# Performance work log

Hardware: AMD Instinct MI355X
Metric: run time of the kernel (lower is better)

## Reference

```python
import jax, jax.numpy as jnp
import numpy as np

B, H, W = 64, 224, 224
EPS = 1e-5


def setup_inputs() -> dict:
    key = jax.random.key(0)
    ks = jax.random.split(key, 8)
    n = lambda k, s, std: jax.random.normal(k, s, jnp.float32) * std
    return {
        "x": jax.random.normal(ks[0], (B, 1, H, W), jnp.float32),
        "conv1_w": n(ks[1], (24, 1, 3, 3), 0.2),
        "conv1_b": jnp.zeros((24,), jnp.float32),
        "bn1_g": jnp.ones((24,), jnp.float32),
        "bn1_b": jnp.zeros((24,), jnp.float32),
        "conv2_w": n(ks[2], (48, 24, 3, 3), 0.07),
        "conv2_b": jnp.zeros((48,), jnp.float32),
        "bn2_g": jnp.ones((48,), jnp.float32),
        "bn2_b": jnp.zeros((48,), jnp.float32),
        "fconv_w": n(ks[3], (48, 48, 56, 56), 0.003),
        "fconv_b": jnp.zeros((48,), jnp.float32),
        "lin1_w": n(ks[4], (24, 48), 0.02),
        "lin1_b": jnp.zeros((24,), jnp.float32),
        "lin2_w": n(ks[5], (4, 24), 0.01),
        "lin2_b": jnp.array([0.0, 0.0, 1.0, 0.0], jnp.float32),  # torch init: identity transform bias
    }


def conv2d(x, w, b):
    y = jax.lax.conv_general_dilated(x, w, (1, 1), ((1, 1), (1, 1)),
                                     dimension_numbers=("NCHW", "OIHW", "NCHW"))
    return y + b[None, :, None, None]


def batchnorm(x, g, b):
    # train-mode BN: batch statistics over (N, H, W), biased variance
    m = x.mean((0, 2, 3), keepdims=True)
    v = x.var((0, 2, 3), keepdims=True)
    return (x - m) * jax.lax.rsqrt(v + EPS) * g[None, :, None, None] + b[None, :, None, None]


def maxpool2(x):
    b, c, h, w = x.shape
    return x.reshape(b, c, h // 2, 2, w // 2, 2).max(axis=(3, 5))


def affine_grid(theta, h, w):
    # theta: [B,2,3]; align_corners=False normalized coords (torch default)
    xs = (jnp.arange(w, dtype=jnp.float32) * 2 + 1) / w - 1.0
    ys = (jnp.arange(h, dtype=jnp.float32) * 2 + 1) / h - 1.0
    gx, gy = jnp.meshgrid(xs, ys)                      # [H,W] each
    base = jnp.stack([gx, gy, jnp.ones_like(gx)], -1)  # [H,W,3] (x, y, 1)
    return jnp.einsum("bij,hwj->bhwi", theta, base)    # [B,H,W,2] -> (x, y)


def grid_sample(img, grid):
    # bilinear, zeros padding, align_corners=False (torch defaults)
    b, c, h, w = img.shape
    ix = ((grid[..., 0] + 1.0) * w - 1.0) * 0.5        # [B,H,W]
    iy = ((grid[..., 1] + 1.0) * h - 1.0) * 0.5
    x0 = jnp.floor(ix); y0 = jnp.floor(iy)
    x1 = x0 + 1.0; y1 = y0 + 1.0
    wx1 = ix - x0; wx0 = 1.0 - wx1
    wy1 = iy - y0; wy0 = 1.0 - wy1
    bidx = jnp.arange(b)[:, None, None]

    def tap(xf, yf, wgt):
        valid = (xf >= 0) & (xf < w) & (yf >= 0) & (yf < h)
        xi = jnp.clip(xf, 0, w - 1).astype(jnp.int32)
        yi = jnp.clip(yf, 0, h - 1).astype(jnp.int32)
        vals = img[bidx, :, yi, xi]                    # [B,H,W,C]
        return vals * (wgt * valid)[..., None]

    out = (tap(x0, y0, wx0 * wy0) + tap(x1, y0, wx1 * wy0)
           + tap(x0, y1, wx0 * wy1) + tap(x1, y1, wx1 * wy1))
    return jnp.transpose(out, (0, 3, 1, 2))            # [B,C,H,W]


def reference(x, conv1_w, conv1_b, bn1_g, bn1_b, conv2_w, conv2_b, bn2_g, bn2_b,
              fconv_w, fconv_b, lin1_w, lin1_b, lin2_w, lin2_b):
    b, _, h, w = x.shape
    x1 = maxpool2(jax.nn.relu(batchnorm(conv2d(x, conv1_w, conv1_b), bn1_g, bn1_b)))
    x1 = maxpool2(jax.nn.relu(batchnorm(conv2d(x1, conv2_w, conv2_b), bn2_g, bn2_b)))
    # final_conv with kernel 56 over a 56x56 map == full contraction
    feat = jnp.einsum("bchw,ochw->bo", x1, fconv_w) + fconv_b      # [B,48]
    theta4 = jax.nn.relu(feat @ lin1_w.T + lin1_b) @ lin2_w.T + lin2_b  # [B,4]
    tx, ty, scale, angle = theta4[:, 0], theta4[:, 1], theta4[:, 2], theta4[:, 3]
    c, s = jnp.cos(angle), jnp.sin(angle)
    # (T @ R @ S)[:, :2] built directly, fully vectorized over batch
    row0 = jnp.stack([scale * c, -scale * s, tx], -1)
    row1 = jnp.stack([scale * s, scale * c, ty], -1)
    theta = jnp.stack([row0, row1], 1)                 # [B,2,3]
    grid = affine_grid(theta, h, w)
    out = grid_sample(x, grid)
    return out, tx, ty, scale, angle
```

## Files before the change

### kernel.cpp

```cpp
#include <hip/hip_runtime.h>
#include <hip/hip_bf16.h>

#define NB 64
#define H0 224
#define W0 224
#define C1 24
#define C2 48
#define H1 112
#define W1 112
#define H2 56
#define W2 56
#define EPSV 1e-5f

#define WS_STATS1   0
#define WS_STATS2   432
#define WS_FEAT     1296
#define WS_B2       4368
#define WS_X2       11280
#define WS_FWT      (WS_X2 + 4818944)
#define WS_X1       9645072
#define WS_NEED_BIG ((size_t)(WS_X1 + 9633792) * 4)
#define OUT0_ELEMS  (NB*H0*W0)

typedef _Float16 v8h __attribute__((ext_vector_type(8)));
typedef float    v4f __attribute__((ext_vector_type(4)));

static __device__ __forceinline__ unsigned short f2h(float v) {
    _Float16 h = (_Float16)v;
    unsigned short us;
    __builtin_memcpy(&us, &h, 2);
    return us;
}

__global__ __launch_bounds__(256) void k_stats_prep(
    const float* __restrict__ x, const float* __restrict__ w1, const float* __restrict__ b1,
    const float* __restrict__ w2, const float* __restrict__ fw,
    float* __restrict__ ws, _Float16* __restrict__ x1g, _Float16* __restrict__ fwt)
{
    __shared__ __align__(16) unsigned char smem[18432];
    const int tid = threadIdx.x;
    const int bid = blockIdx.x;

    if (bid >= 3136) {
        _Float16 (*T)[136] = (_Float16(*)[136])smem;
        const int p = bid - 3136;
        if (p < 54) {
            int t = p * 256 + tid;
            if (t >= 432 && t < WS_B2) ws[t] = 0.f;
            if (t < 13824) {
                int e = t & 7;
                int l = (t >> 3) & 63;
                int g = t >> 9;
                int q = l >> 4, ml = l & 15;
                int kp = g / 3, nt = g % 3;
                int ic = q * 8 + e;
                int oc = nt * 16 + ml;
                float v = (ic < C1) ? w2[(oc * C1 + ic) * 9 + kp] : 0.f;
                ((_Float16*)(ws + WS_B2))[t] = (_Float16)v;
            }
        }
        const int kb = p * 128;
#pragma unroll
        for (int t3 = 0; t3 < 6; t3++) {
            int li = tid + 256 * t3;
            int o = li >> 5, k4 = li & 31;
            float4 v = *(const float4*)&fw[(long)o * 150528 + kb + 4 * k4];
            T[o][4 * k4 + 0] = (_Float16)v.x;
            T[o][4 * k4 + 1] = (_Float16)v.y;
            T[o][4 * k4 + 2] = (_Float16)v.z;
            T[o][4 * k4 + 3] = (_Float16)v.w;
        }
        __syncthreads();
        uint4* dst = (uint4*)&fwt[(long)kb * 48];
#pragma unroll
        for (int t3 = 0; t3 < 3; t3++) {
            int u = tid + 256 * t3;
            int gg = u / 384;
            int rem = u % 384;
            int o = rem >> 3;
            int k8 = (rem & 7) * 8;
            dst[u] = *(const uint4*)&T[o][gg * 64 + k8];
        }
        return;
    }

    float (*xt)[36] = (float(*)[36])smem;
    unsigned int (*outt)[13] = (unsigned int(*)[13])(smem + 4896);
    float* sred = (float*)(smem + 18208);

    const int b = bid / 49;
    const int rem0 = bid % 49;
    const int py0 = (rem0 / 7) * 16, px0 = (rem0 % 7) * 16;
    const int iy0 = 2 * py0 - 1, ix0 = 2 * px0 - 1;
    const float* xb = x + b * (H0 * W0);

    for (int li = tid; li < 34 * 34; li += 256) {
        int ry = li / 34, rx = li % 34;
        int gy = iy0 + ry, gx = ix0 + rx;
        bool ok = (gy >= 0) & (gy < H0) & (gx >= 0) & (gx < W0);
        xt[ry][rx] = ok ? xb[gy * W0 + gx] : 0.f;
    }

    const int wid = tid >> 6;
    const int lane = tid & 63;
    const int c0 = wid * 6;

    const int c0s = __builtin_amdgcn_readfirstlane(c0);
    const float* __restrict__ wps = w1 + c0s * 9;
    float wr[54], br[6];
#pragma unroll
    for (int k = 0; k < 54; k++) wr[k] = wps[k];
#pragma unroll
    for (int c = 0; c < 6; c++) br[c] = b1[c0s + c];

    __syncthreads();

    float s[6] = {0.f, 0.f, 0.f, 0.f, 0.f, 0.f};
    float q[6] = {0.f, 0.f, 0.f, 0.f, 0.f, 0.f};
    const int pc = lane & 15;
    const int pr0 = lane >> 4;

#pragma unroll
    for (int pp = 0; pp < 4; pp++) {
        const int pr = pr0 + 4 * pp;
        float patch[16];
#pragma unroll
        for (int i2 = 0; i2 < 4; i2++)
#pragma unroll
            for (int j2 = 0; j2 < 4; j2++)
                patch[i2 * 4 + j2] = xt[2 * pr + i2][2 * pc + j2];

        unsigned int pk[3];
#pragma unroll
        for (int cp = 0; cp < 3; cp++) {
            unsigned int pv = 0;
#pragma unroll
            for (int h = 0; h < 2; h++) {
                int c = 2 * cp + h;
                float m4 = -1e30f;
#pragma unroll
                for (int sy = 0; sy < 2; sy++)
#pragma unroll
                    for (int sx = 0; sx < 2; sx++) {
                        float a = br[c];
#pragma unroll
                        for (int ky = 0; ky < 3; ky++)
#pragma unroll
                            for (int kx = 0; kx < 3; kx++)
                                a = fmaf(patch[(sy + ky) * 4 + (sx + kx)], wr[c * 9 + ky * 3 + kx], a);
                        s[c] += a;
                        q[c] = fmaf(a, a, q[c]);
                        m4 = fmaxf(m4, a);
                    }
                pv |= ((unsigned int)f2h(m4)) << (16 * h);
            }
            pk[cp] = pv;
        }
        int pos = pr * 16 + pc;
        outt[pos][wid * 3 + 0] = pk[0];
        outt[pos][wid * 3 + 1] = pk[1];
        outt[pos][wid * 3 + 2] = pk[2];
    }

#pragma unroll
    for (int c = 0; c < 6; c++) {
#pragma unroll
        for (int off = 32; off > 0; off >>= 1) {
            s[c] += __shfl_down(s[c], off, 64);
            q[c] += __shfl_down(q[c], off, 64);
        }
    }
    if (lane == 0) {
#pragma unroll
        for (int c = 0; c < 6; c++) {
            sred[c0 + c] = s[c];
            sred[C1 + c0 + c] = q[c];
        }
    }
    __syncthreads();

    if (tid < 2 * C1) {
        atomicAdd(&ws[WS_STATS1 + (bid & 7) * 2 * C1 + tid], sred[tid]);
    }

    for (int u = tid; u < 768; u += 256) {
        int pos = u / 3, prt = u % 3;
        int pr = pos >> 4, pcc = pos & 15;
        long p = (long)(b * H1 + (py0 + pr)) * W1 + (px0 + pcc);
        uint4 v;
        v.x = outt[pos][4 * prt + 0];
        v.y = outt[pos][4 * prt + 1];
        v.z = outt[pos][4 * prt + 2];
        v.w = outt[pos][4 * prt + 3];
        *(uint4*)(x1g + p * C1 + prt * 8) = v;
    }
}

__global__ __launch_bounds__(256, 2) void k_conv2_fused6(
    const _Float16* __restrict__ x1g, const _Float16* __restrict__ bpp,
    const float* __restrict__ g1, const float* __restrict__ bb1,
    const float* __restrict__ b2,
    float* __restrict__ ws, unsigned int* __restrict__ pooltu)
{
    __shared__ __align__(16) _Float16 x1t[2][18][18][32];
    __shared__ float alds[C1], bflds[C1];
    __shared__ float sred[2 * C2];

    const int tid = threadIdx.x;
    const int w = tid >> 6;
    const int lane = tid & 63;
    const int ml = lane & 15;
    const int qq = lane >> 4;

    v8h B[9][3];
#pragma unroll
    for (int kp = 0; kp < 9; kp++)
#pragma unroll
        for (int nt = 0; nt < 3; nt++)
            B[kp][nt] = *(const v8h*)&bpp[((kp * 3 + nt) * 64 + lane) * 8];

    if (tid < C1) {
        float s = 0.f, q = 0.f;
#pragma unroll
        for (int i = 0; i < 8; i++) {
            s += ws[WS_STATS1 + i * 2 * C1 + tid];
            q += ws[WS_STATS1 + i * 2 * C1 + C1 + tid];
        }
        const float N = (float)(NB * H0 * W0);
        float m = s / N;
        float v = q / N - m * m;
        float a = g1[tid] / sqrtf(v + EPSV);
        alds[tid] = a;
        bflds[tid] = bb1[tid] - m * a;
    }
    if (tid < 2 * C2) sred[tid] = 0.f;

    {
        v8h z8;
#pragma unroll
        for (int e = 0; e < 8; e++) z8[e] = (_Float16)0.f;
        for (int li = tid; li < 2 * 18 * 18; li += 256) {
            int bu = li / 324, pos = li % 324;
            *(v8h*)&x1t[bu][pos / 18][pos % 18][24] = z8;
        }
    }

    float bias[3] = {b2[ml], b2[16 + ml], b2[32 + ml]};

    int spart[4], spr[4], spc[4]; bool sv[4];
#pragma unroll
    for (int s4 = 0; s4 < 4; s4++) {
        int li = tid + s4 * 256;
        sv[s4] = li < 972;
        int part = li % 3;
        int pos = li / 3;
        spart[s4] = part;
        spr[s4] = pos / 18;
        spc[s4] = pos % 18;
    }

    const int nb = gridDim.x;
    const int NTILE = 3136;
    int qn = NTILE / nb, rn = NTILE % nb;
    int start = (blockIdx.x < rn) ? blockIdx.x * (qn + 1)
                                  : rn * (qn + 1) + (blockIdx.x - rn) * qn;
    int cnt = (blockIdx.x < rn) ? qn + 1 : qn;

    float svacc[3] = {0.f, 0.f, 0.f}, qvacc[3] = {0.f, 0.f, 0.f};

    v8h raw[4];
    bool inb_n[4];
    {
        int t = start;
        int tb = t / 49, rem = t % 49;
        int ty = (rem / 7) * 16, txx = (rem % 7) * 16;
#pragma unroll
        for (int s4 = 0; s4 < 4; s4++) {
#pragma unroll
            for (int e = 0; e < 8; e++) raw[s4][e] = (_Float16)0.f;
            int gy = ty - 1 + spr[s4], gx = txx - 1 + spc[s4];
            inb_n[s4] = sv[s4] & (gy >= 0) & (gy < H1) & (gx >= 0) & (gx < W1);
            if (inb_n[s4])
                raw[s4] = *(const v8h*)&x1g[((tb * H1 + gy) * W1 + gx) * C1 + spart[s4] * 8];
        }
    }
    __syncthreads();

#pragma unroll
    for (int s4 = 0; s4 < 4; s4++) {
        if (sv[s4]) {
            v8h r8;
            if (inb_n[s4]) {
#pragma unroll
                for (int e = 0; e < 8; e++) {
                    int c = spart[s4] * 8 + e;
                    float vv = fmaxf(fmaf((float)raw[s4][e], alds[c], bflds[c]), 0.f);
                    r8[e] = (_Float16)vv;
                }
            } else {
#pragma unroll
                for (int e = 0; e < 8; e++) r8[e] = (_Float16)0.f;
            }
            *(v8h*)&x1t[0][spr[s4]][spc[s4]][spart[s4] * 8] = r8;
        }
    }
    __syncthreads();

    for (int it = 0; it < cnt; it++) {
        const int cur = it & 1;
        const int t = start + it;
        const int tb = t / 49, rem = t % 49;
        const int ty = (rem / 7) * 16, txx = (rem % 7) * 16;

        const bool haveNext = (it + 1 < cnt);
        if (haveNext) {
            int t2 = t + 1;
            int nb2 = t2 / 49, rem2 = t2 % 49;
            int ny = (rem2 / 7) * 16, nx = (rem2 % 7) * 16;
#pragma unroll
            for (int s4 = 0; s4 < 4; s4++) {
#pragma unroll
                for (int e = 0; e < 8; e++) raw[s4][e] = (_Float16)0.f;
                int gy = ny - 1 + spr[s4], gx = nx - 1 + spc[s4];
                inb_n[s4] = sv[s4] & (gy >= 0) & (gy < H1) & (gx >= 0) & (gx < W1);
                if (inb_n[s4])
                    raw[s4] = *(const v8h*)&x1g[((nb2 * H1 + gy) * W1 + gx) * C1 + spart[s4] * 8];
            }
        }

        v4f acc[4][3];
#pragma unroll
        for (int mt = 0; mt < 4; mt++)
#pragma unroll
            for (int nt = 0; nt < 3; nt++)
                acc[mt][nt] = (v4f){0.f, 0.f, 0.f, 0.f};

#pragma unroll
        for (int kp = 0; kp < 9; kp++) {
            const int ky = kp / 3, kx = kp % 3;
#pragma unroll
            for (int mt = 0; mt < 4; mt++) {
                const int r = 4 * w + mt;
                v8h a = *(const v8h*)&x1t[cur][r + ky][ml + kx][qq * 8];
                acc[mt][0] = __builtin_amdgcn_mfma_f32_16x16x32_f16(a, B[kp][0], acc[mt][0], 0, 0, 0);
                acc[mt][1] = __builtin_amdgcn_mfma_f32_16x16x32_f16(a, B[kp][1], acc[mt][1], 0, 0, 0);
                acc[mt][2] = __builtin_amdgcn_mfma_f32_16x16x32_f16(a, B[kp][2], acc[mt][2], 0, 0, 0);
            }
        }

#pragma unroll
        for (int nt = 0; nt < 3; nt++) {
            int oc = nt * 16 + ml;
            float z[4][4];
#pragma unroll
            for (int mt = 0; mt < 4; mt++)
#pragma unroll
                for (int rg = 0; rg < 4; rg++) {
                    float val = acc[mt][nt][rg] + bias[nt];
                    z[mt][rg] = val;
                    svacc[nt] += val;
                    qvacc[nt] = fmaf(val, val, qvacc[nt]);
                }
#pragma unroll
            for (int h = 0; h < 2; h++) {
                int py = (ty >> 1) + 2 * w + h;
                float m0 = fmaxf(fmaxf(z[2 * h][0], z[2 * h][1]),
                                 fmaxf(z[2 * h + 1][0], z[2 * h + 1][1]));
                float m1 = fmaxf(fmaxf(z[2 * h][2], z[2 * h][3]),
                                 fmaxf(z[2 * h + 1][2], z[2 * h + 1][3]));
                int px0 = (txx >> 1) + qq * 2;
                int k = oc * 3136 + py * W2 + px0;
                unsigned int pk2 = (unsigned int)f2h(m0) | ((unsigned int)f2h(m1) << 16);
                pooltu[(((k >> 6) * NB + tb) << 5) + ((k & 63) >> 1)] = pk2;
            }
        }

        if (haveNext) {
#pragma unroll
            for (int s4 = 0; s4 < 4; s4++) {
                if (sv[s4]) {
                    v8h r8;
                    if (inb_n[s4]) {
#pragma unroll
                        for (int e = 0; e < 8; e++) {
                            int c = spart[s4] * 8 + e;
                            float vv = fmaxf(fmaf((float)raw[s4][e], alds[c], bflds[c]), 0.f);
                            r8[e] = (_Float16)vv;
                        }
                    } else {
#pragma unroll
                        for (int e = 0; e < 8; e++) r8[e] = (_Float16)0.f;
                    }
                    *(v8h*)&x1t[cur ^ 1][spr[s4]][spc[s4]][spart[s4] * 8] = r8;
                }
            }
        }
        __syncthreads();
    }

#pragma unroll
    for (int nt = 0; nt < 3; nt++) {
        float sv2 = svacc[nt], qv = qvacc[nt];
        sv2 += __shfl_xor(sv2, 16, 64); qv += __shfl_xor(qv, 16, 64);
        sv2 += __shfl_xor(sv2, 32, 64); qv += __shfl_xor(qv, 32, 64);
        if (qq == 0) {
            atomicAdd(&sred[nt * 16 + ml], sv2);
            atomicAdd(&sred[C2 + nt * 16 + ml], qv);
        }
    }
    __syncthreads();
    if (tid < 2 * C2) {
        atomicAdd(&ws[WS_STATS2 + (blockIdx.x & 7) * 2 * C2 + tid], sred[tid]);
    }
}

__global__ __launch_bounds__(256) void k_fconv6(
    const unsigned int* __restrict__ pooltu, const _Float16* __restrict__ fwt,
    const float* __restrict__ ws, const float* __restrict__ g2, const float* __restrict__ bb2,
    float* __restrict__ feat)
{
    __shared__ __align__(16) _Float16 fwh[48][136];
    __shared__ __align__(16) _Float16 x2h[64][136];
    __shared__ float csh[2 * C2];

    const int tid = threadIdx.x;
    const int bx = blockIdx.x;

    const uint4* fsrc = (const uint4*)fwt + (long)bx * 768;
    const uint4* psrc = (const uint4*)pooltu + (long)bx * 1024;
    uint4 fr[3], pr[4];
#pragma unroll
    for (int t3 = 0; t3 < 3; t3++) fr[t3] = fsrc[tid + 256 * t3];
#pragma unroll
    for (int t4 = 0; t4 < 4; t4++) pr[t4] = psrc[tid + 256 * t4];

    if (tid < C2) {
        int c = tid;
        float s = 0.f, q = 0.f;
#pragma unroll
        for (int i = 0; i < 8; i++) {
            s += ws[WS_STATS2 + i * 2 * C2 + c];
            q += ws[WS_STATS2 + i * 2 * C2 + C2 + c];
        }
        const float N = (float)(NB * H1 * W1);
        float m = s / N;
        float v = q / N - m * m;
        float a = g2[c] / sqrtf(v + EPSV);
        csh[c] = a;
        csh[C2 + c] = bb2[c] - m * a;
    }
    __syncthreads();

#pragma unroll
    for (int t3 = 0; t3 < 3; t3++) {
        int li = tid + 256 * t3;
        int gg = li / 384;
        int o = (li % 384) / 8;
        int kin = (li & 7) * 8;
        *(uint4*)&fwh[o][gg * 64 + kin] = fr[t3];
    }
    const int c0 = (2 * bx) / 49, c1 = (2 * bx + 1) / 49;
    const float a0 = csh[c0], bf0 = csh[C2 + c0];
    const float a1 = csh[c1], bf1 = csh[C2 + c1];
#pragma unroll
    for (int t4 = 0; t4 < 4; t4++) {
        int li = tid + 256 * t4;
        int gg = li >> 9;
        int b = (li & 511) >> 3;
        int kin = (li & 7) * 8;
        float aa = gg ? a1 : a0;
        float bb = gg ? bf1 : bf0;
        union { uint4 u; v8h h; } cv;
        cv.u = pr[t4];
        v8h r8;
#pragma unroll
        for (int e = 0; e < 8; e++)
            r8[e] = (_Float16)fmaxf(fmaf((float)cv.h[e], aa, bb), 0.f);
        *(v8h*)&x2h[b][gg * 64 + kin] = r8;
    }
    __syncthreads();

    const int w = tid >> 6;
    const int lane = tid & 63;
    const int ml = lane & 15;
    const int qq = lane >> 4;

    v4f acc[3];
#pragma unroll
    for (int ot = 0; ot < 3; ot++) acc[ot] = (v4f){0.f, 0.f, 0.f, 0.f};

#pragma unroll
    for (int ks = 0; ks < 4; ks++) {
        v8h a = *(const v8h*)&x2h[w * 16 + ml][ks * 32 + qq * 8];
#pragma unroll
        for (int ot = 0; ot < 3; ot++) {
            v8h bb = *(const v8h*)&fwh[ot * 16 + ml][ks * 32 + qq * 8];
            acc[ot] = __builtin_amdgcn_mfma_f32_16x16x32_f16(a, bb, acc[ot], 0, 0, 0);
        }
    }

#pragma unroll
    for (int ot = 0; ot < 3; ot++)
#pragma unroll
        for (int rg = 0; rg < 4; rg++)
            atomicAdd(&feat[(w * 16 + qq * 4 + rg) * C2 + ot * 16 + ml], acc[ot][rg]);
}

__global__ __launch_bounds__(256) void k_sample4(
    const float* __restrict__ x, const float* __restrict__ feat, const float* __restrict__ fcb,
    const float* __restrict__ l1w, const float* __restrict__ l1b,
    const float* __restrict__ l2w, const float* __restrict__ l2b,
    float* __restrict__ out)
{
    __shared__ float hsh[24];
    __shared__ float th[4];
    const int b = blockIdx.y;
    const int tid = threadIdx.x;
    if (tid < 24) {
        float a = l1b[tid];
#pragma unroll
        for (int o = 0; o < C2; o++)
            a = fmaf(feat[b * C2 + o] + fcb[o], l1w[tid * C2 + o], a);
        hsh[tid] = fmaxf(a, 0.f);
    }
    __syncthreads();
    if (tid < 4) {
        float a = l2b[tid];
#pragma unroll
        for (int jj = 0; jj < 24; jj++) a = fmaf(hsh[jj], l2w[tid * 24 + jj], a);
        th[tid] = a;
        if (blockIdx.x == 0) out[OUT0_ELEMS + tid * NB + b] = a;
    }
    __syncthreads();

    const float tx = th[0], ty = th[1], sc = th[2], an = th[3];
    const float cc = cosf(an), ss = sinf(an);
    const float t00 = sc * cc, t01 = -sc * ss, t10 = sc * ss, t11 = sc * cc;
    const float* xb = x + b * (H0 * W0);

    int idx = (blockIdx.x * 256 + tid) * 2;
    int i = idx / W0, j = idx % W0;
    float ys = (2.f * (float)i + 1.f) / (float)H0 - 1.f;

    float o2[2];
#pragma unroll
    for (int px = 0; px < 2; px++) {
        float xs = (2.f * (float)(j + px) + 1.f) / (float)W0 - 1.f;
        float gx = t00 * xs + t01 * ys + tx;
        float gy = t10 * xs + t11 * ys + ty;
        float ix = ((gx + 1.f) * (float)W0 - 1.f) * 0.5f;
        float iy = ((gy + 1.f) * (float)H0 - 1.f) * 0.5f;
        float x0 = floorf(ix), y0 = floorf(iy);
        float x1f = x0 + 1.f, y1f = y0 + 1.f;
        float wx1 = ix - x0, wx0 = 1.f - wx1;
        float wy1 = iy - y0, wy0 = 1.f - wy1;
        auto tap = [&](float xf, float yf, float wgt) -> float {
            bool valid = (xf >= 0.f) & (xf < (float)W0) & (yf >= 0.f) & (yf < (float)H0);
            int xi = (int)fminf(fmaxf(xf, 0.f), (float)(W0 - 1));
            int yi = (int)fminf(fmaxf(yf, 0.f), (float)(H0 - 1));
            return valid ? xb[yi * W0 + xi] * wgt : 0.f;
        };
        o2[px] = tap(x0, y0, wx0 * wy0) + tap(x1f, y0, wx1 * wy0)
               + tap(x0, y1f, wx0 * wy1) + tap(x1f, y1f, wx1 * wy1);
    }
    *(float2*)&out[(b * H0 + i) * W0 + j] = make_float2(o2[0], o2[1]);
}

__global__ __launch_bounds__(256) void k_init(const float* __restrict__ w2, float* __restrict__ ws)
{
    int t = blockIdx.x * 256 + threadIdx.x;
    if (t < WS_B2) ws[t] = 0.f;
    if (t < 13824) {
        int e = t & 7;
        int l = (t >> 3) & 63;
        int g = t >> 9;
        int q = l >> 4, ml = l & 15;
        int kp = g / 3, nt = g % 3;
        int ic = q * 8 + e;
        int oc = nt * 16 + ml;
        float v = (ic < C1) ? w2[(oc * C1 + ic) * 9 + kp] : 0.f;
        ((_Float16*)(ws + WS_B2))[t] = (_Float16)v;
    }
}

__global__ __launch_bounds__(256) void k_conv1_stats(
    const float* __restrict__ x, const float* __restrict__ w1, const float* __restrict__ b1,
    float* __restrict__ ws)
{
    float s[C1], q[C1];
#pragma unroll
    for (int c = 0; c < C1; c++) { s[c] = 0.f; q[c] = 0.f; }
    const int NT = gridDim.x * 256;
    const int total = NB * H0 * W0;
    for (int p = blockIdx.x * 256 + threadIdx.x; p < total; p += NT) {
        int b = p / (H0 * W0);
        int r = p % (H0 * W0);
        int y = r / W0;
        int xx = r % W0;
        const float* xb = x + b * (H0 * W0);
        float patch[9];
#pragma unroll
        for (int dy = 0; dy < 3; dy++)
#pragma unroll
            for (int dx = 0; dx < 3; dx++) {
                int yy = y + dy - 1, xc = xx + dx - 1;
                bool ok = (yy >= 0) & (yy < H0) & (xc >= 0) & (xc < W0);
                patch[dy * 3 + dx] = ok ? xb[yy * W0 + xc] : 0.f;
            }
#pragma unroll
        for (int c = 0; c < C1; c++) {
            const float* wp = w1 + c * 9;
            float a = b1[c];
#pragma unroll
            for (int k = 0; k < 9; k++) a = fmaf(patch[k], wp[k], a);
            s[c] += a;
            q[c] = fmaf(a, a, q[c]);
        }
    }
#pragma unroll
    for (int c = 0; c < C1; c++) {
#pragma unroll
        for (int off = 32; off > 0; off >>= 1) {
            s[c] += __shfl_down(s[c], off, 64);
            q[c] += __shfl_down(q[c], off, 64);
        }
    }
    __shared__ float sred[2 * C1];
    if (threadIdx.x < 2 * C1) sred[threadIdx.x] = 0.f;
    __syncthreads();
    if ((threadIdx.x & 63) == 0) {
#pragma unroll
        for (int c = 0; c < C1; c++) {
            atomicAdd(&sred[c], s[c]);
            atomicAdd(&sred[C1 + c], q[c]);
        }
    }
    __syncthreads();
    if (threadIdx.x < 2 * C1) {
        atomicAdd(&ws[WS_STATS1 + (blockIdx.x & 7) * 2 * C1 + threadIdx.x], sred[threadIdx.x]);
    }
}

__global__ __launch_bounds__(256, 2) void k_conv2_fused(
    const float* __restrict__ x, const float* __restrict__ w1, const float* __restrict__ b1,
    const float* __restrict__ g1, const float* __restrict__ bb1,
    const _Float16* __restrict__ bpp, const float* __restrict__ b2,
    float* __restrict__ ws, float* __restrict__ pool)
{
    __shared__ float xt[22][38];
    __shared__ __align__(16) _Float16 x1t[10][18][32];
    __shared__ __align__(16) _Float16 Blds[13824];
    __shared__ float wlds[C1 * 9];
    __shared__ float blds[C1], alds[C1], bflds[C1];
    __shared__ float sred[2 * C2];

    const int tid = threadIdx.x;
    const int b = blockIdx.z;
    const int y0 = blockIdx.y * 8;
    const int x0 = blockIdx.x * 16;
    const float* xb = x + b * (H0 * W0);

    for (int li = tid; li < 13824 / 8; li += 256)
        ((uint4*)Blds)[li] = ((const uint4*)bpp)[li];

    if (tid < C1 * 9) wlds[tid] = w1[tid];
    if (tid < C1) {
        float s = 0.f, q = 0.f;
#pragma unroll
        for (int i = 0; i < 8; i++) {
            s += ws[WS_STATS1 + i * 2 * C1 + tid];
            q += ws[WS_STATS1 + i * 2 * C1 + C1 + tid];
        }
        const float N = (float)(NB * H0 * W0);
        float m = s / N;
        float v = q / N - m * m;
        float a = g1[tid] / sqrtf(v + EPSV);
        blds[tid] = b1[tid];
        alds[tid] = a;
        bflds[tid] = bb1[tid] - m * a;
    }
    if (tid < 2 * C2) sred[tid] = 0.f;

    const int oy0 = 2 * y0 - 3, ox0 = 2 * x0 - 3;
    for (int li = tid; li < 22 * 38; li += 256) {
        int ry = li / 38, rx = li % 38;
        int gy = oy0 + ry, gx = ox0 + rx;
        bool ok = (gy >= 0) & (gy < H0) & (gx >= 0) & (gx < W0);
        xt[ry][rx] = ok ? xb[gy * W0 + gx] : 0.f;
    }
    __syncthreads();

    if (tid < 180) {
        int pr = tid / 18, pc = tid % 18;
        int gy = y0 - 1 + pr, gx = x0 - 1 + pc;
        bool valid = (gy >= 0) & (gy < H1) & (gx >= 0) & (gx < W1);
        float patch[16];
#pragma unroll
        for (int dy = 0; dy < 4; dy++)
#pragma unroll
            for (int dx = 0; dx < 4; dx++)
                patch[dy * 4 + dx] = xt[2 * pr + dy][2 * pc + dx];
        unsigned int* dst = (unsigned int*)&x1t[pr][pc][0];
#pragma unroll
        for (int cp = 0; cp < 12; cp++) {
            unsigned int pk = 0;
#pragma unroll
            for (int h = 0; h < 2; h++) {
                int c = 2 * cp + h;
                float m4 = -1e30f;
#pragma unroll
                for (int py = 0; py < 2; py++)
#pragma unroll
                    for (int px = 0; px < 2; px++) {
                        float a = blds[c];
#pragma unroll
                        for (int ky = 0; ky < 3; ky++)
#pragma unroll
                            for (int kx = 0; kx < 3; kx++)
                                a = fmaf(patch[(py + ky) * 4 + (px + kx)], wlds[c * 9 + ky * 3 + kx], a);
                        m4 = fmaxf(m4, fmaf(a, alds[c], bflds[c]));
                    }
                float v = valid ? fmaxf(m4, 0.f) : 0.f;
                pk |= ((unsigned int)f2h(v)) << (16 * h);
            }
            dst[cp] = pk;
        }
        dst[12] = 0; dst[13] = 0; dst[14] = 0; dst[15] = 0;
    }
    __syncthreads();

    const int w = tid >> 6;
    const int lane = tid & 63;
    const int ml = lane & 15;
    const int q = lane >> 4;

    v4f acc[2][3];
#pragma unroll
    for (int mt = 0; mt < 2; mt++)
#pragma unroll
        for (int nt = 0; nt < 3; nt++)
            acc[mt][nt] = (v4f){0.f, 0.f, 0.f, 0.f};

#pragma unroll
    for (int kp = 0; kp < 9; kp++) {
        const int ky = kp / 3, kx = kp % 3;
        v8h B0 = *(const v8h*)&Blds[((kp * 3 + 0) * 64 + lane) * 8];
        v8h B1 = *(const v8h*)&Blds[((kp * 3 + 1) * 64 + lane) * 8];
        v8h B2 = *(const v8h*)&Blds[((kp * 3 + 2) * 64 + lane) * 8];
#pragma unroll
        for (int mt = 0; mt < 2; mt++) {
            const int r = 2 * w + mt;
            v8h a = *(const v8h*)&x1t[r + ky][ml + kx][q * 8];
            acc[mt][0] = __builtin_amdgcn_mfma_f32_16x16x32_f16(a, B0, acc[mt][0], 0, 0, 0);
            acc[mt][1] = __builtin_amdgcn_mfma_f32_16x16x32_f16(a, B1, acc[mt][1], 0, 0, 0);
            acc[mt][2] = __builtin_amdgcn_mfma_f32_16x16x32_f16(a, B2, acc[mt][2], 0, 0, 0);
        }
    }

#pragma unroll
    for (int nt = 0; nt < 3; nt++) {
        int oc = nt * 16 + ml;
        float bias = b2[oc];
        float z[2][4];
        float sv = 0.f, qv = 0.f;
#pragma unroll
        for (int mt = 0; mt < 2; mt++)
#pragma unroll
            for (int rg = 0; rg < 4; rg++) {
                float val = acc[mt][nt][rg] + bias;
                z[mt][rg] = val;
                sv += val;
                qv = fmaf(val, val, qv);
            }
        sv += __shfl_xor(sv, 16, 64); qv += __shfl_xor(qv, 16, 64);
        sv += __shfl_xor(sv, 32, 64); qv += __shfl_xor(qv, 32, 64);
        if (q == 0) { atomicAdd(&sred[oc], sv); atomicAdd(&sred[C2 + oc], qv); }

        int py = (y0 >> 1) + w;
#pragma unroll
        for (int j = 0; j < 2; j++) {
            float m = fmaxf(fmaxf(z[0][2 * j], z[0][2 * j + 1]),
                            fmaxf(z[1][2 * j], z[1][2 * j + 1]));
            int px = (x0 >> 1) + q * 2 + j;
            pool[((b * C2 + oc) * H2 + py) * W2 + px] = m;
        }
    }
    __syncthreads();
    if (tid < 2 * C2) {
        int cp = (blockIdx.x + 7 * blockIdx.y + 31 * blockIdx.z) & 7;
        atomicAdd(&ws[WS_STATS2 + cp * 2 * C2 + tid], sred[tid]);
    }
}

#define KC 512
#define KSUB 128
__global__ __launch_bounds__(256) void k_fconv(
    const float* __restrict__ pool, const float* __restrict__ ws,
    const float* __restrict__ g2, const float* __restrict__ bb2,
    const float* __restrict__ fw, float* __restrict__ feat)
{
    __shared__ float fwt[C2][KSUB + 1];
    __shared__ float x2t[NB][KSUB + 1];
    __shared__ float csh[2 * C2];
    if (threadIdx.x < C2) {
        int c = threadIdx.x;
        float s = 0.f, q = 0.f;
#pragma unroll
        for (int i = 0; i < 8; i++) {
            s += ws[WS_STATS2 + i * 2 * C2 + c];
            q += ws[WS_STATS2 + i * 2 * C2 + C2 + c];
        }
        const float N = (float)(NB * H1 * W1);
        float m = s / N;
        float v = q / N - m * m;
        float a = g2[c] / sqrtf(v + EPSV);
        csh[c] = a;
        csh[C2 + c] = bb2[c] - m * a;
    }
    int k0 = blockIdx.x * KC;
    int i = threadIdx.x / 16, j = threadIdx.x % 16;
    float acc[3][4] = {{0.f}};
    for (int sub = 0; sub < KC / KSUB; sub++) {
        int kb = k0 + sub * KSUB;
        __syncthreads();
        for (int li = threadIdx.x; li < C2 * KSUB; li += 256) {
            int o = li / KSUB, k = li % KSUB;
            fwt[o][k] = fw[o * 150528 + kb + k];
        }
        for (int li = threadIdx.x; li < NB * KSUB; li += 256) {
            int b = li / KSUB, k = li % KSUB;
            int kk = kb + k;
            int c = kk / (H2 * W2);
            float v = pool[b * 150528 + kk];
            x2t[b][k] = fmaxf(fmaf(v, csh[c], csh[C2 + c]), 0.f);
        }
        __syncthreads();
        for (int k = 0; k < KSUB; k++) {
            float fa[3], xv[4];
#pragma unroll
            for (int c = 0; c < 3; c++) fa[c] = fwt[i + 16 * c][k];
#pragma unroll
            for (int d = 0; d < 4; d++) xv[d] = x2t[j + 16 * d][k];
#pragma unroll
            for (int c = 0; c < 3; c++)
#pragma unroll
                for (int d = 0; d < 4; d++)
                    acc[c][d] = fmaf(fa[c], xv[d], acc[c][d]);
        }
    }
#pragma unroll
    for (int c = 0; c < 3; c++)
#pragma unroll
        for (int d = 0; d < 4; d++)
            atomicAdd(&feat[(j + 16 * d) * C2 + (i + 16 * c)], acc[c][d]);
}

__global__ __launch_bounds__(256) void k_sample(
    const float* __restrict__ x, const float* __restrict__ feat, const float* __restrict__ fcb,
    const float* __restrict__ l1w, const float* __restrict__ l1b,
    const float* __restrict__ l2w, const float* __restrict__ l2b,
    float* __restrict__ out)
{
    __shared__ float hsh[24];
    __shared__ float th[4];
    int b = blockIdx.y;
    int tid = threadIdx.x;
    if (tid < 24) {
        float a = l1b[tid];
        for (int o = 0; o < C2; o++)
            a = fmaf(feat[b * C2 + o] + fcb[o], l1w[tid * C2 + o], a);
        hsh[tid] = fmaxf(a, 0.f);
    }
    __syncthreads();
    if (tid < 4) {
        float a = l2b[tid];
        for (int jj = 0; jj < 24; jj++) a = fmaf(hsh[jj], l2w[tid * 24 + jj], a);
        th[tid] = a;
        if (blockIdx.x == 0) out[OUT0_ELEMS + tid * NB + b] = a;
    }
    __syncthreads();

    int idx = blockIdx.x * 256 + tid;
    int i = idx / W0, j = idx % W0;
    float tx = th[0], ty = th[1], sc = th[2], an = th[3];
    float cc = cosf(an), ss = sinf(an);
    float t00 = sc * cc, t01 = -sc * ss, t10 = sc * ss, t11 = sc * cc;
    float xs = (2.f * (float)j + 1.f) / (float)W0 - 1.f;
    float ys = (2.f * (float)i + 1.f) / (float)H0 - 1.f;
    float gx = t00 * xs + t01 * ys + tx;
    float gy = t10 * xs + t11 * ys + ty;
    float ix = ((gx + 1.f) * (float)W0 - 1.f) * 0.5f;
    float iy = ((gy + 1.f) * (float)H0 - 1.f) * 0.5f;
    float x0 = floorf(ix), y0 = floorf(iy);
    float x1f = x0 + 1.f, y1f = y0 + 1.f;
    float wx1 = ix - x0, wx0 = 1.f - wx1;
    float wy1 = iy - y0, wy0 = 1.f - wy1;
    const float* xb = x + b * (H0 * W0);
    auto tap = [&](float xf, float yf, float wgt) -> float {
        bool valid = (xf >= 0.f) & (xf < (float)W0) & (yf >= 0.f) & (yf < (float)H0);
        int xi = (int)fminf(fmaxf(xf, 0.f), (float)(W0 - 1));
        int yi = (int)fminf(fmaxf(yf, 0.f), (float)(H0 - 1));
        return valid ? xb[yi * W0 + xi] * wgt : 0.f;
    };
    float o = tap(x0, y0, wx0 * wy0) + tap(x1f, y0, wx1 * wy0)
            + tap(x0, y1f, wx0 * wy1) + tap(x1f, y1f, wx1 * wy1);
    out[(b * H0 + i) * W0 + j] = o;
}

extern "C" void kernel_launch(void* const* d_in, const int* in_sizes, int n_in,
                              void* d_out, int out_size, void* d_ws, size_t ws_size,
                              hipStream_t stream)
{
    const float* x    = (const float*)d_in[0];
    const float* c1w  = (const float*)d_in[1];
    const float* c1b  = (const float*)d_in[2];
    const float* bn1g = (const float*)d_in[3];
    const float* bn1b = (const float*)d_in[4];
    const float* c2w  = (const float*)d_in[5];
    const float* c2b  = (const float*)d_in[6];
    const float* bn2g = (const float*)d_in[7];
    const float* bn2b = (const float*)d_in[8];
    const float* fw   = (const float*)d_in[9];
    const float* fcb  = (const float*)d_in[10];
    const float* l1w  = (const float*)d_in[11];
    const float* l1b  = (const float*)d_in[12];
    const float* l2w  = (const float*)d_in[13];
    const float* l2b  = (const float*)d_in[14];
    float* ws  = (float*)d_ws;
    float* out = (float*)d_out;

    if (ws_size >= WS_NEED_BIG) {
        hipMemsetAsync(ws, 0, 432 * sizeof(float), stream);
        k_stats_prep<<<dim3(4312), 256, 0, stream>>>(
            x, c1w, c1b, c2w, fw, ws, (_Float16*)(ws + WS_X1), (_Float16*)(ws + WS_FWT));
        k_conv2_fused6<<<dim3(512), 256, 0, stream>>>(
            (const _Float16*)(ws + WS_X1), (const _Float16*)(ws + WS_B2),
            bn1g, bn1b, c2b, ws, (unsigned int*)(ws + WS_X2));
        k_fconv6<<<dim3(1176), 256, 0, stream>>>(
            (const unsigned int*)(ws + WS_X2), (const _Float16*)(ws + WS_FWT),
            ws, bn2g, bn2b, ws + WS_FEAT);
        k_sample4<<<dim3(98, 64), 256, 0, stream>>>(
            x, ws + WS_FEAT, fcb, l1w, l1b, l2w, l2b, out);
    } else {
        k_init<<<dim3(54), 256, 0, stream>>>(c2w, ws);
        k_conv1_stats<<<dim3(1024), 256, 0, stream>>>(x, c1w, c1b, ws);
        k_conv2_fused<<<dim3(7, 14, 64), 256, 0, stream>>>(
            x, c1w, c1b, bn1g, bn1b, (const _Float16*)(ws + WS_B2), c2b, ws, ws + WS_X2);
        k_fconv<<<dim3(150528 / KC), 256, 0, stream>>>(ws + WS_X2, ws, bn2g, bn2b, fw, ws + WS_FEAT);
        k_sample<<<dim3(196, 64), 256, 0, stream>>>(x, ws + WS_FEAT, fcb, l1w, l1b, l2w, l2b, out);
    }
}
```

Baseline: 218.9 us.

## Retile conv1 kernel to full-width 16-row strips processed in two chunks

Result: slower. 253.8 us (+15.9%).

```diff
diff --git a/kernel.cpp b/kernel.cpp
--- a/kernel.cpp
+++ b/kernel.cpp
@@ -32,18 +32,18 @@
     return us;
 }
 
-__global__ __launch_bounds__(256) void k_stats_prep(
+__global__ __launch_bounds__(256) void k_stats_prep2(
     const float* __restrict__ x, const float* __restrict__ w1, const float* __restrict__ b1,
     const float* __restrict__ w2, const float* __restrict__ fw,
     float* __restrict__ ws, _Float16* __restrict__ x1g, _Float16* __restrict__ fwt)
 {
-    __shared__ __align__(16) unsigned char smem[18432];
+    __shared__ __align__(16) unsigned char smem[39808];
     const int tid = threadIdx.x;
     const int bid = blockIdx.x;
 
-    if (bid >= 3136) {
+    if (bid >= 896) {
         _Float16 (*T)[136] = (_Float16(*)[136])smem;
-        const int p = bid - 3136;
+        const int p = bid - 896;
         if (p < 54) {
             int t = p * 256 + tid;
             if (t >= 432 && t < WS_B2) ws[t] = 0.f;
@@ -84,19 +84,18 @@
         return;
     }
 
-    float (*xt)[36] = (float(*)[36])smem;
-    unsigned int (*outt)[13] = (unsigned int(*)[13])(smem + 4896);
-    float* sred = (float*)(smem + 18208);
-
-    const int b = bid / 49;
-    const int rem0 = bid % 49;
-    const int py0 = (rem0 / 7) * 16, px0 = (rem0 % 7) * 16;
-    const int iy0 = 2 * py0 - 1, ix0 = 2 * px0 - 1;
+    float (*xt)[226] = (float(*)[226])smem;
+    unsigned int (*outt)[13] = (unsigned int(*)[13])(smem + 16272);
+    float* sred = (float*)(smem + 39568);
+
+    const int b = bid / 14;
+    const int rg = bid % 14;
+    const int iy0 = 16 * rg - 1;
     const float* xb = x + b * (H0 * W0);
 
-    for (int li = tid; li < 34 * 34; li += 256) {
-        int ry = li / 34, rx = li % 34;
-        int gy = iy0 + ry, gx = ix0 + rx;
+    for (int li = tid; li < 18 * 226; li += 256) {
+        int ry = li / 226, rx = li % 226;
+        int gy = iy0 + ry, gx = rx - 1;
         bool ok = (gy >= 0) & (gy < H0) & (gx >= 0) & (gx < W0);
         xt[ry][rx] = ok ? xb[gy * W0 + gx] : 0.f;
     }
@@ -117,49 +116,66 @@
 
     float s[6] = {0.f, 0.f, 0.f, 0.f, 0.f, 0.f};
     float q[6] = {0.f, 0.f, 0.f, 0.f, 0.f, 0.f};
-    const int pc = lane & 15;
-    const int pr0 = lane >> 4;
-
-#pragma unroll
-    for (int pp = 0; pp < 4; pp++) {
-        const int pr = pr0 + 4 * pp;
-        float patch[16];
-#pragma unroll
-        for (int i2 = 0; i2 < 4; i2++)
-#pragma unroll
-            for (int j2 = 0; j2 < 4; j2++)
-                patch[i2 * 4 + j2] = xt[2 * pr + i2][2 * pc + j2];
-
-        unsigned int pk[3];
-#pragma unroll
-        for (int cp = 0; cp < 3; cp++) {
-            unsigned int pv = 0;
-#pragma unroll
-            for (int h = 0; h < 2; h++) {
-                int c = 2 * cp + h;
-                float m4 = -1e30f;
-#pragma unroll
-                for (int sy = 0; sy < 2; sy++)
-#pragma unroll
-                    for (int sx = 0; sx < 2; sx++) {
-                        float a = br[c];
-#pragma unroll
-                        for (int ky = 0; ky < 3; ky++)
-#pragma unroll
-                            for (int kx = 0; kx < 3; kx++)
-                                a = fmaf(patch[(sy + ky) * 4 + (sx + kx)], wr[c * 9 + ky * 3 + kx], a);
-                        s[c] += a;
-                        q[c] = fmaf(a, a, q[c]);
-                        m4 = fmaxf(m4, a);
-                    }
-                pv |= ((unsigned int)f2h(m4)) << (16 * h);
+
+#pragma unroll
+    for (int chunk = 0; chunk < 2; chunk++) {
+#pragma unroll
+        for (int pp = 0; pp < 7; pp++) {
+            const int pos = lane + 64 * pp;
+            const int prl = pos / 112, pc = pos % 112;
+            const int xr0 = 8 * chunk + 2 * prl;
+            float patch[16];
+#pragma unroll
+            for (int i2 = 0; i2 < 4; i2++)
+#pragma unroll
+                for (int j2 = 0; j2 < 4; j2++)
+                    patch[i2 * 4 + j2] = xt[xr0 + i2][2 * pc + j2];
+
+            unsigned int pk[3];
+#pragma unroll
+            for (int cp = 0; cp < 3; cp++) {
+                unsigned int pv = 0;
+#pragma unroll
+                for (int h = 0; h < 2; h++) {
+                    int c = 2 * cp + h;
+                    float m4 = -1e30f;
+#pragma unroll
+                    for (int sy = 0; sy < 2; sy++)
+#pragma unroll
+                        for (int sx = 0; sx < 2; sx++) {
+                            float a = br[c];
+#pragma unroll
+                            for (int ky = 0; ky < 3; ky++)
+#pragma unroll
+                                for (int kx = 0; kx < 3; kx++)
+                                    a = fmaf(patch[(sy + ky) * 4 + (sx + kx)], wr[c * 9 + ky * 3 + kx], a);
+                            s[c] += a;
+                            q[c] = fmaf(a, a, q[c]);
+                            m4 = fmaxf(m4, a);
+                        }
+                    pv |= ((unsigned int)f2h(m4)) << (16 * h);
+                }
+                pk[cp] = pv;
             }
-            pk[cp] = pv;
-        }
-        int pos = pr * 16 + pc;
-        outt[pos][wid * 3 + 0] = pk[0];
-        outt[pos][wid * 3 + 1] = pk[1];
-        outt[pos][wid * 3 + 2] = pk[2];
+            outt[pos][wid * 3 + 0] = pk[0];
+            outt[pos][wid * 3 + 1] = pk[1];
+            outt[pos][wid * 3 + 2] = pk[2];
+        }
+        __syncthreads();
+
+        for (int u = tid; u < 1344; u += 256) {
+            int pos = u / 3, prt = u % 3;
+            int prl = pos / 112, pc = pos % 112;
+            int py = 8 * rg + 4 * chunk + prl;
+            long p = (long)(b * H1 + py) * W1 + pc;
+            uint4 v;
+            v.x = outt[pos][4 * prt + 0];
+            v.y = outt[pos][4 * prt + 1];
+            v.z = outt[pos][4 * prt + 2];
+            v.w = outt[pos][4 * prt + 3];
+            *(uint4*)(x1g + p * C1 + prt * 8) = v;
+        }
+        __syncthreads();
     }
 
 #pragma unroll
@@ -178,21 +194,8 @@
         }
     }
     __syncthreads();
-
     if (tid < 2 * C1) {
         atomicAdd(&ws[WS_STATS1 + (bid & 7) * 2 * C1 + tid], sred[tid]);
-    }
-
-    for (int u = tid; u < 768; u += 256) {
-        int pos = u / 3, prt = u % 3;
-        int pr = pos >> 4, pcc = pos & 15;
-        long p = (long)(b * H1 + (py0 + pr)) * W1 + (px0 + pcc);
-        uint4 v;
-        v.x = outt[pos][4 * prt + 0];
-        v.y = outt[pos][4 * prt + 1];
-        v.z = outt[pos][4 * prt + 2];
-        v.w = outt[pos][4 * prt + 3];
-        *(uint4*)(x1g + p * C1 + prt * 8) = v;
     }
 }
 
@@ -931,7 +934,7 @@
 
     if (ws_size >= WS_NEED_BIG) {
         hipMemsetAsync(ws, 0, 432 * sizeof(float), stream);
-        k_stats_prep<<<dim3(4312), 256, 0, stream>>>(
+        k_stats_prep2<<<dim3(2072), 256, 0, stream>>>(
             x, c1w, c1b, c2w, fw, ws, (_Float16*)(ws + WS_X1), (_Float16*)(ws + WS_FWT));
         k_conv2_fused6<<<dim3(512), 256, 0, stream>>>(
             (const _Float16*)(ws + WS_X1), (const _Float16*)(ws + WS_B2),
```
